# Kernel tuning notes

Measured on AMD Instinct MI355X. Metric: run time of the kernel, lower is better.

Reference implementation:

```python
import math
import jax, jax.numpy as jnp
import numpy as np

NUM_HEADS = 8
ATTN_STD = np.array([1.0, 2.0, 4.0, 8.0, 1.0, 2.0, 4.0, 8.0], dtype=np.float32)
ATTN_OFFSET = np.array([-1.0, -2.0, -4.0, -8.0, -1.0, -2.0, -4.0, -8.0], dtype=np.float32)


def setup_inputs() -> dict:
    key = jax.random.key(0)
    k1, k2, k3 = jax.random.split(key, 3)
    B, L, D = 2, 2048, 1024
    values = jax.random.normal(k1, (B, L, D), dtype=jnp.float32)
    # learned params (init_std = 0.02, matching nn.init.normal_)
    input_weights = 0.02 * jax.random.normal(k2, (D, D), dtype=jnp.float32)
    output_weight = 0.02 * jax.random.normal(k3, (D, D), dtype=jnp.float32)
    return {"values": values, "input_weights": input_weights, "output_weight": output_weight}


def _gaussian_attn_weights(qlen, dtype):
    # Faithful closed form of get_attn_cache retrieval for offsets <= -1:
    # w[h, q, k] = N(k - q - offset_h; std_h), no renormalization, no mask.
    stds = jnp.asarray(ATTN_STD, dtype=dtype)[:, None, None]      # [H,1,1]
    offs = jnp.asarray(ATTN_OFFSET, dtype=dtype)[:, None, None]   # [H,1,1]
    q = jnp.arange(qlen, dtype=dtype)[None, :, None]               # [1,L,1]
    k = jnp.arange(qlen, dtype=dtype)[None, None, :]               # [1,1,L]
    dist = k - q - offs                                            # [H,L,L]
    inv_norm = 1.0 / (stds * math.sqrt(2.0 * math.pi))
    return inv_norm * jnp.exp(-0.5 * (dist / stds) ** 2)           # [H,L,L]


def reference(values, input_weights, output_weight):
    B, L, D = values.shape
    H = NUM_HEADS
    pd = D // H
    # project(): F.linear(values, input_weights) then split into heads
    v = values @ input_weights.T                                   # [B,L,D]
    v = v.reshape(B, L, H, pd).transpose(0, 2, 1, 3)               # [B,H,L,pd]
    probs = _gaussian_attn_weights(L, values.dtype)                # [H,L,L]
    attended = jnp.einsum('hqk,bhkd->bhqd', probs, v)              # [B,H,L,pd]
    attended = attended.transpose(0, 2, 1, 3).reshape(B, L, D)     # merge heads
    # output_projection (Linear, no bias)
    return attended @ output_weight.T
```

## Files before the change

kernel.cpp:

```cpp
#include <hip/hip_runtime.h>
#include <hip/hip_bf16.h>

#define L_SEQ   2048
#define D_MODEL 1024
#define B_SZ    2
#define LP      (L_SEQ + 192)
#define PADF    96

typedef __attribute__((ext_vector_type(8))) short bf16x8;
typedef __attribute__((ext_vector_type(4))) float f32x4;

__device__ __forceinline__ void gll16(const void* g, void* l) {
    __builtin_amdgcn_global_load_lds(
        (const __attribute__((address_space(1))) unsigned int*)(g),
        (__attribute__((address_space(3))) unsigned int*)(l),
        16, 0, 0);
}

__device__ __forceinline__ ushort bf16_hi(float x) {
    __hip_bfloat16 h = __float2bfloat16(x);
    return *reinterpret_cast<ushort*>(&h);
}
__device__ __forceinline__ float bf16_back(ushort u) {
    __hip_bfloat16 h = *reinterpret_cast<__hip_bfloat16*>(&u);
    return __bfloat162float(h);
}

__global__ __launch_bounds__(256) void split_mat(const float* __restrict__ in,
                                                 ushort* __restrict__ hi,
                                                 ushort* __restrict__ lo)
{
    const size_t i = ((size_t)blockIdx.x * 256 + threadIdx.x) * 4;
    float4 v = *(const float4*)(in + i);
    float f[4] = {v.x, v.y, v.z, v.w};
    ushort hb[4], lb[4];
    #pragma unroll
    for (int j = 0; j < 4; ++j) {
        hb[j] = bf16_hi(f[j]);
        lb[j] = bf16_hi(f[j] - bf16_back(hb[j]));
    }
    *(ushort4*)(hi + i) = make_ushort4(hb[0], hb[1], hb[2], hb[3]);
    *(ushort4*)(lo + i) = make_ushort4(lb[0], lb[1], lb[2], lb[3]);
}

__global__ __launch_bounds__(256) void zero_pads(float* __restrict__ vpad)
{
    const int r  = blockIdx.x / 96;
    const int rr = blockIdx.x % 96;
    const int b  = r >> 1;
    const int row0 = (r & 1) ? (LP - 96) : 0;
    size_t off = ((size_t)b * LP + row0 + rr) * D_MODEL + threadIdx.x * 4;
    *(float4*)(vpad + off) = make_float4(0.f, 0.f, 0.f, 0.f);
}

template<int DO_PAD>
__global__ __launch_bounds__(512) void gemm_split(const ushort* __restrict__ Ah,
                                                  const ushort* __restrict__ Al,
                                                  const ushort* __restrict__ Bh,
                                                  const ushort* __restrict__ Bl,
                                                  float* __restrict__ C)
{
    __shared__ __align__(16) ushort lds[2][4][128 * 32];

    const int tid = threadIdx.x;
    const int w   = tid >> 6;
    const int l   = tid & 63;

    const int xcd = blockIdx.x & 7;
    const int idx = blockIdx.x >> 3;
    const int bm  = (xcd * 4 + (idx >> 3)) * 128;
    const int bn  = (idx & 7) * 128;

    const int srow   = tid >> 2;
    const int schunk = (tid & 3) ^ ((tid >> 3) & 3);
    const ushort* gAh = Ah + (size_t)(bm + srow) * 1024 + schunk * 8;
    const ushort* gAl = Al + (size_t)(bm + srow) * 1024 + schunk * 8;
    const ushort* gBh = Bh + (size_t)(bn + srow) * 1024 + schunk * 8;
    const ushort* gBl = Bl + (size_t)(bn + srow) * 1024 + schunk * 8;
    const int ldst = tid * 8;

    const int fr  = l & 15;
    const int fq  = l >> 4;
    const int swz = (fr >> 1) & 3;
    const int rdo = (fq ^ swz) << 3;
    const int wr  = w >> 2;
    const int wc  = w & 3;

    f32x4 acc[4][2];
    #pragma unroll
    for (int mi = 0; mi < 4; ++mi)
        #pragma unroll
        for (int ni = 0; ni < 2; ++ni) acc[mi][ni] = (f32x4){0.f, 0.f, 0.f, 0.f};

    #define STAGE(buf, kt)                                        \
        do {                                                      \
            const size_t ko_ = (size_t)(kt) * 32;                 \
            gll16(gAh + ko_, &lds[(buf)][0][ldst]);               \
            gll16(gAl + ko_, &lds[(buf)][1][ldst]);               \
            gll16(gBh + ko_, &lds[(buf)][2][ldst]);               \
            gll16(gBl + ko_, &lds[(buf)][3][ldst]);               \
        } while (0)

    STAGE(0, 0);
    __syncthreads();

    for (int kt = 0; kt < 32; ++kt) {
        const int cur = kt & 1;
        if (kt + 1 < 32) STAGE(cur ^ 1, kt + 1);

        bf16x8 ah[4], al[4];
        #pragma unroll
        for (int mi = 0; mi < 4; ++mi) {
            const int row = wr * 64 + mi * 16 + fr;
            ah[mi] = *(const bf16x8*)&lds[cur][0][row * 32 + rdo];
            al[mi] = *(const bf16x8*)&lds[cur][1][row * 32 + rdo];
        }
        #pragma unroll
        for (int ni = 0; ni < 2; ++ni) {
            const int row = wc * 32 + ni * 16 + fr;
            bf16x8 bh = *(const bf16x8*)&lds[cur][2][row * 32 + rdo];
            bf16x8 bl = *(const bf16x8*)&lds[cur][3][row * 32 + rdo];
            #pragma unroll
            for (int mi = 0; mi < 4; ++mi)
                acc[mi][ni] = __builtin_amdgcn_mfma_f32_16x16x32_bf16(ah[mi], bh, acc[mi][ni], 0, 0, 0);
            #pragma unroll
            for (int mi = 0; mi < 4; ++mi)
                acc[mi][ni] = __builtin_amdgcn_mfma_f32_16x16x32_bf16(al[mi], bh, acc[mi][ni], 0, 0, 0);
            #pragma unroll
            for (int mi = 0; mi < 4; ++mi)
                acc[mi][ni] = __builtin_amdgcn_mfma_f32_16x16x32_bf16(ah[mi], bl, acc[mi][ni], 0, 0, 0);
        }
        __syncthreads();
    }
    #undef STAGE

    #pragma unroll
    for (int mi = 0; mi < 4; ++mi) {
        #pragma unroll
        for (int ni = 0; ni < 2; ++ni) {
            const int col = bn + wc * 32 + ni * 16 + fr;
            #pragma unroll
            for (int j = 0; j < 4; ++j) {
                const int m = bm + wr * 64 + mi * 16 + fq * 4 + j;
                const size_t row = DO_PAD ? ((size_t)(m >> 11) * LP + (m & (L_SEQ - 1)) + PADF)
                                          : (size_t)m;
                C[row * 1024 + col] = acc[mi][ni][j];
            }
        }
    }
}

__global__ __launch_bounds__(256) void gauss_conv_split(const float* __restrict__ vpad,
                                                        ushort* __restrict__ Oh,
                                                        ushort* __restrict__ Ol)
{
    __shared__ __align__(16) float xs[256 * 64];
    __shared__ float wt[128];

    const int tid = threadIdx.x;
    const int d0  = blockIdx.x * 64;
    const int q0  = blockIdx.y * 128;
    const int b   = blockIdx.z;
    const int h   = blockIdx.x >> 1;

    if (tid < 128) {
        const float sig = (float)(1 << (h & 3));
        const float t = ((float)(tid - 71) + sig) / sig;
        wt[tid] = (0.39894228040143267794f / sig) * expf(-0.5f * t * t);
    }

    const float* src = vpad + ((size_t)b * LP + (PADF - 71) + q0) * 1024 + d0;
    #pragma unroll
    for (int p = 0; p < 16; ++p) {
        const int f   = p * 256 + tid;
        const int row = f >> 4;
        const int c4  = (f & 15) * 4;
        gll16(src + (size_t)row * 1024 + c4, &xs[f * 4]);
    }
    __syncthreads();

    const int d     = tid & 63;
    const int qbase = (tid >> 6) * 32;

    float acc[32];
    #pragma unroll
    for (int qq = 0; qq < 32; ++qq) acc[qq] = 0.f;

    #pragma unroll 1
    for (int c = 0; c < 8; ++c) {
        float xw[47];
        const float* xp = &xs[(qbase + c * 16) * 64 + d];
        #pragma unroll
        for (int j = 0; j < 47; ++j) xw[j] = xp[j * 64];
        #pragma unroll
        for (int dd = 0; dd < 16; ++dd) {
            const float wv = wt[c * 16 + dd];
            #pragma unroll
            for (int qq = 0; qq < 32; ++qq)
                acc[qq] = fmaf(wv, xw[dd + qq], acc[qq]);
        }
    }

    ushort* oh = Oh + ((size_t)b * L_SEQ + q0 + qbase) * 1024 + d0 + d;
    ushort* ol = Ol + ((size_t)b * L_SEQ + q0 + qbase) * 1024 + d0 + d;
    #pragma unroll
    for (int qq = 0; qq < 32; ++qq) {
        const ushort hv = bf16_hi(acc[qq]);
        oh[(size_t)qq * 1024] = hv;
        ol[(size_t)qq * 1024] = bf16_hi(acc[qq] - bf16_back(hv));
    }
}

extern "C" void kernel_launch(void* const* d_in, const int* in_sizes, int n_in,
                              void* d_out, int out_size, void* d_ws, size_t ws_size,
                              hipStream_t stream)
{
    const float* values = (const float*)d_in[0];
    const float* w_in   = (const float*)d_in[1];
    const float* w_out  = (const float*)d_in[2];
    float* out = (float*)d_out;

    float*  vpad = (float*)d_ws;
    ushort* Ph = (ushort*)(vpad + (size_t)B_SZ * LP * D_MODEL);
    ushort* Pl = Ph + (size_t)4096 * 1024;
    ushort* Wh = Pl + (size_t)4096 * 1024;
    ushort* Wl = Wh + (size_t)1024 * 1024;

    split_mat<<<dim3(4096), dim3(256), 0, stream>>>(values, Ph, Pl);
    split_mat<<<dim3(1024), dim3(256), 0, stream>>>(w_in, Wh, Wl);
    zero_pads<<<dim3(4 * 96), dim3(256), 0, stream>>>(vpad);

    gemm_split<1><<<dim3(256), dim3(512), 0, stream>>>(Ph, Pl, Wh, Wl, vpad);

    dim3 cgrid(D_MODEL / 64, L_SEQ / 128, B_SZ);
    gauss_conv_split<<<cgrid, dim3(256), 0, stream>>>(vpad, Ph, Pl);

    split_mat<<<dim3(1024), dim3(256), 0, stream>>>(w_out, Wh, Wl);
    gemm_split<0><<<dim3(256), dim3(512), 0, stream>>>(Ph, Pl, Wh, Wl, out);
}
```

Before: 162.4 us.

## Deepen GEMM LDS pipeline to four stages and fuse weight splitting

```diff
diff --git a/kernel.cpp b/kernel.cpp
--- a/kernel.cpp
+++ b/kernel.cpp
@@ -41,6 +41,30 @@
     }
     *(ushort4*)(hi + i) = make_ushort4(hb[0], hb[1], hb[2], hb[3]);
     *(ushort4*)(lo + i) = make_ushort4(lb[0], lb[1], lb[2], lb[3]);
+}
+
+__global__ __launch_bounds__(256) void split_w(const float* __restrict__ w_in,
+                                               const float* __restrict__ w_out,
+                                               ushort* __restrict__ Wh,
+                                               ushort* __restrict__ Wl,
+                                               ushort* __restrict__ W2h,
+                                               ushort* __restrict__ W2l)
+{
+    const int sel = blockIdx.x >> 10;
+    const float* src = sel ? w_out : w_in;
+    ushort* oh = sel ? W2h : Wh;
+    ushort* ol = sel ? W2l : Wl;
+    const size_t i = ((size_t)(blockIdx.x & 1023) * 256 + threadIdx.x) * 4;
+    float4 v = *(const float4*)(src + i);
+    float f[4] = {v.x, v.y, v.z, v.w};
+    ushort hb[4], lb[4];
+    #pragma unroll
+    for (int j = 0; j < 4; ++j) {
+        hb[j] = bf16_hi(f[j]);
+        lb[j] = bf16_hi(f[j] - bf16_back(hb[j]));
+    }
+    *(ushort4*)(oh + i) = make_ushort4(hb[0], hb[1], hb[2], hb[3]);
+    *(ushort4*)(ol + i) = make_ushort4(lb[0], lb[1], lb[2], lb[3]);
 }
 
 __global__ __launch_bounds__(256) void zero_pads(float* __restrict__ vpad)
@@ -60,7 +84,7 @@
                                                   const ushort* __restrict__ Bl,
                                                   float* __restrict__ C)
 {
-    __shared__ __align__(16) ushort lds[2][4][128 * 32];
+    __shared__ __align__(16) ushort lds[4][4][128 * 32];
 
     const int tid = threadIdx.x;
     const int w   = tid >> 6;
@@ -101,38 +125,50 @@
             gll16(gBl + ko_, &lds[(buf)][3][ldst]);               \
         } while (0)
 
+    #define WAITBAR(N) asm volatile("s_waitcnt vmcnt(" #N ")\n\ts_barrier" ::: "memory")
+
+    #define COMPUTE(cur)                                                                   \
+        do {                                                                               \
+            bf16x8 ah[4], al[4];                                                           \
+            _Pragma("unroll")                                                              \
+            for (int mi = 0; mi < 4; ++mi) {                                               \
+                const int row = wr * 64 + mi * 16 + fr;                                    \
+                ah[mi] = *(const bf16x8*)&lds[(cur)][0][row * 32 + rdo];                   \
+                al[mi] = *(const bf16x8*)&lds[(cur)][1][row * 32 + rdo];                   \
+            }                                                                              \
+            _Pragma("unroll")                                                              \
+            for (int ni = 0; ni < 2; ++ni) {                                               \
+                const int row = wc * 32 + ni * 16 + fr;                                    \
+                bf16x8 bh = *(const bf16x8*)&lds[(cur)][2][row * 32 + rdo];                \
+                bf16x8 bl = *(const bf16x8*)&lds[(cur)][3][row * 32 + rdo];                \
+                _Pragma("unroll")                                                          \
+                for (int mi = 0; mi < 4; ++mi)                                             \
+                    acc[mi][ni] = __builtin_amdgcn_mfma_f32_16x16x32_bf16(ah[mi], bh, acc[mi][ni], 0, 0, 0); \
+                _Pragma("unroll")                                                          \
+                for (int mi = 0; mi < 4; ++mi)                                             \
+                    acc[mi][ni] = __builtin_amdgcn_mfma_f32_16x16x32_bf16(al[mi], bh, acc[mi][ni], 0, 0, 0); \
+                _Pragma("unroll")                                                          \
+                for (int mi = 0; mi < 4; ++mi)                                             \
+                    acc[mi][ni] = __builtin_amdgcn_mfma_f32_16x16x32_bf16(ah[mi], bl, acc[mi][ni], 0, 0, 0); \
+            }                                                                              \
+        } while (0)
+
     STAGE(0, 0);
-    __syncthreads();
-
-    for (int kt = 0; kt < 32; ++kt) {
-        const int cur = kt & 1;
-        if (kt + 1 < 32) STAGE(cur ^ 1, kt + 1);
-
-        bf16x8 ah[4], al[4];
-        #pragma unroll
-        for (int mi = 0; mi < 4; ++mi) {
-            const int row = wr * 64 + mi * 16 + fr;
-            ah[mi] = *(const bf16x8*)&lds[cur][0][row * 32 + rdo];
-            al[mi] = *(const bf16x8*)&lds[cur][1][row * 32 + rdo];
-        }
-        #pragma unroll
-        for (int ni = 0; ni < 2; ++ni) {
-            const int row = wc * 32 + ni * 16 + fr;
-            bf16x8 bh = *(const bf16x8*)&lds[cur][2][row * 32 + rdo];
-            bf16x8 bl = *(const bf16x8*)&lds[cur][3][row * 32 + rdo];
-            #pragma unroll
-            for (int mi = 0; mi < 4; ++mi)
-                acc[mi][ni] = __builtin_amdgcn_mfma_f32_16x16x32_bf16(ah[mi], bh, acc[mi][ni], 0, 0, 0);
-            #pragma unroll
-            for (int mi = 0; mi < 4; ++mi)
-                acc[mi][ni] = __builtin_amdgcn_mfma_f32_16x16x32_bf16(al[mi], bh, acc[mi][ni], 0, 0, 0);
-            #pragma unroll
-            for (int mi = 0; mi < 4; ++mi)
-                acc[mi][ni] = __builtin_amdgcn_mfma_f32_16x16x32_bf16(ah[mi], bl, acc[mi][ni], 0, 0, 0);
-        }
-        __syncthreads();
-    }
+    STAGE(1, 1);
+    STAGE(2, 2);
+
+    for (int kt = 0; kt < 29; ++kt) {
+        WAITBAR(8);
+        STAGE((kt + 3) & 3, kt + 3);
+        COMPUTE(kt & 3);
+    }
+    WAITBAR(8); COMPUTE(1);
+    WAITBAR(4); COMPUTE(2);
+    WAITBAR(0); COMPUTE(3);
+
     #undef STAGE
+    #undef WAITBAR
+    #undef COMPUTE
 
     #pragma unroll
     for (int mi = 0; mi < 4; ++mi) {
@@ -221,13 +257,15 @@
     float* out = (float*)d_out;
 
     float*  vpad = (float*)d_ws;
-    ushort* Ph = (ushort*)(vpad + (size_t)B_SZ * LP * D_MODEL);
-    ushort* Pl = Ph + (size_t)4096 * 1024;
-    ushort* Wh = Pl + (size_t)4096 * 1024;
-    ushort* Wl = Wh + (size_t)1024 * 1024;
+    ushort* Ph  = (ushort*)(vpad + (size_t)B_SZ * LP * D_MODEL);
+    ushort* Pl  = Ph  + (size_t)4096 * 1024;
+    ushort* Wh  = Pl  + (size_t)4096 * 1024;
+    ushort* Wl  = Wh  + (size_t)1024 * 1024;
+    ushort* W2h = Wl  + (size_t)1024 * 1024;
+    ushort* W2l = W2h + (size_t)1024 * 1024;
 
     split_mat<<<dim3(4096), dim3(256), 0, stream>>>(values, Ph, Pl);
-    split_mat<<<dim3(1024), dim3(256), 0, stream>>>(w_in, Wh, Wl);
+    split_w<<<dim3(2048), dim3(256), 0, stream>>>(w_in, w_out, Wh, Wl, W2h, W2l);
     zero_pads<<<dim3(4 * 96), dim3(256), 0, stream>>>(vpad);
 
     gemm_split<1><<<dim3(256), dim3(512), 0, stream>>>(Ph, Pl, Wh, Wl, vpad);
@@ -235,6 +273,5 @@
     dim3 cgrid(D_MODEL / 64, L_SEQ / 128, B_SZ);
     gauss_conv_split<<<cgrid, dim3(256), 0, stream>>>(vpad, Ph, Pl);
 
-    split_mat<<<dim3(1024), dim3(256), 0, stream>>>(w_out, Wh, Wl);
-    gemm_split<0><<<dim3(256), dim3(512), 0, stream>>>(Ph, Pl, Wh, Wl, out);
-}
+    gemm_split<0><<<dim3(256), dim3(512), 0, stream>>>(Ph, Pl, W2h, W2l, out);
+}
```

Result: faster. 153.2 us (-5.7%).
